# Kernel optimization log

Hardware: AMD Instinct MI355X
Metric: run time of the kernel (lower is better)

Reference implementation:

```python
import jax, jax.numpy as jnp
import numpy as np

H = 1024
IN = 512
B = 32
E_H = 0.5
Z_MIN = 0.001
Z_MAX = 0.1
DT = 1.0


def setup_inputs() -> dict:
    key = jax.random.key(0)
    ks = jax.random.split(key, 10)
    s = 1.0 / np.sqrt(H)
    uni = lambda k, shape: jax.random.uniform(k, shape, jnp.float32, -s, s)
    return {
        "x": jax.random.normal(ks[0], (IN, B), jnp.float32),
        "h": jax.random.uniform(ks[1], (B, H), jnp.float32),      # hidden state [B,H]
        "X": jnp.ones((B, H, H), jnp.float32),                     # resources
        "U": jnp.full((B, H, H), 0.9, jnp.float32),                # utilization (init 0.9)
        "c_x": uni(ks[2], (H, H)),
        "c_u": uni(ks[3], (H, H)),
        "c_U": uni(ks[4], (H, H)),
        "c_h": uni(ks[5], (H, 1)),
        "w": uni(ks[6], (H, H)),
        "p": uni(ks[7], (H, IN)),
        "b": uni(ks[8], (H, 1)),
    }


def reference(x, h, X, U, c_x, c_u, c_U, c_h, w, p, b):
    sig = jax.nn.sigmoid
    hb = h[:, :, None]                                  # h[b,j] broadcast over k -> [B,H,1]
    # resource (X) update: z_x + (1-z_x)*X - dt*U*X*h
    z_x = Z_MIN + (Z_MAX - Z_MIN) * sig(c_x)            # [H,H]
    X_new = z_x + (1.0 - z_x) * X - DT * U * (X * hb)   # [B,H,H]
    # utilization (U) update, clamped to [Ucap (detached), 1]
    z_u = Z_MIN + (Z_MAX - Z_MIN) * sig(c_u)            # [H,H]
    Ucap = 0.9 * sig(c_U)                               # [H,H]
    U_new = Ucap * z_u + (1.0 - z_u) * U + DT * Ucap * ((1.0 - U) * hb)
    U_new = jnp.clip(U_new, jax.lax.stop_gradient(Ucap), 1.0)
    # hidden update with dynamic weights W = w * U * X (per batch)
    z_h = E_H * sig(c_h)                                # [H,1]
    W = w * U_new * X_new                               # [B,H,H]
    rec = jnp.einsum("bjk,bk->jb", W, h)               # [H,B]
    pre = rec + p @ x + b                               # [H,B]
    h_newT = (1.0 - z_h) * h.T + z_h * sig(pre)         # [H,B]
    return h_newT.T                                     # [B,H]
```

## Files before the change

kernel.cpp:

```cpp
#include <hip/hip_runtime.h>

#define HH 1024
#define INW 512
#define BB 32
#define Z_MIN_C 0.001f
#define Z_RANGE_C 0.099f
#define E_H_C 0.5f

__device__ __forceinline__ float sigmoidf_(float v) {
    return 1.0f / (1.0f + __expf(-v));
}

__global__ __launch_bounds__(256) void stp_fused(
    const float* __restrict__ x,
    const float* __restrict__ h,
    const float* __restrict__ X,
    const float* __restrict__ U,
    const float* __restrict__ c_x,
    const float* __restrict__ c_u,
    const float* __restrict__ c_U,
    const float* __restrict__ c_h,
    const float* __restrict__ w,
    const float* __restrict__ p,
    const float* __restrict__ bias,
    float* __restrict__ out)
{
    const int j = blockIdx.x;
    const int t = threadIdx.x;
    const int lane = t & 63;
    const int wave = t >> 6;

    __shared__ float px_part[8][BB];
    __shared__ float rec_part[BB][4];

    {
        const int b_id = t & 31;
        const int seg = t >> 5;
        float acc = 0.0f;
        const float* prow = p + j * INW + seg * 64;
        const float* xcol = x + seg * 64 * BB + b_id;
        #pragma unroll 8
        for (int i = 0; i < 64; ++i)
            acc += prow[i] * xcol[i * BB];
        px_part[seg][b_id] = acc;
    }

    const int k0 = t * 4;
    float4 cx4 = *(const float4*)(c_x + j * HH + k0);
    float4 cu4 = *(const float4*)(c_u + j * HH + k0);
    float4 cC4 = *(const float4*)(c_U + j * HH + k0);
    float4 wv4 = *(const float4*)(w + j * HH + k0);
    const float* cxv = &cx4.x;
    const float* cuv = &cu4.x;
    const float* cCv = &cC4.x;
    const float* wvv = &wv4.x;

    float zx[4], ozx[4], Acoef[4], ozu[4], Uc[4], wr[4];
    #pragma unroll
    for (int c = 0; c < 4; ++c) {
        float zxx = Z_MIN_C + Z_RANGE_C * sigmoidf_(cxv[c]);
        float zuu = Z_MIN_C + Z_RANGE_C * sigmoidf_(cuv[c]);
        float ucc = 0.9f * sigmoidf_(cCv[c]);
        zx[c] = zxx;
        ozx[c] = 1.0f - zxx;
        ozu[c] = 1.0f - zuu;
        Uc[c] = ucc;
        Acoef[c] = ucc * zuu;
        wr[c] = wvv[c];
    }

    for (int b = 0; b < BB; ++b) {
        const float hj = h[b * HH + j];
        float4 hk4 = *(const float4*)(h + b * HH + k0);
        const int rowbase = (b * HH + j) * HH;
        float4 Xv4 = *(const float4*)(X + rowbase + k0);
        float4 Uv4 = *(const float4*)(U + rowbase + k0);
        const float* Xv = &Xv4.x;
        const float* Uv = &Uv4.x;
        const float* hk = &hk4.x;

        float s = 0.0f;
        #pragma unroll
        for (int c = 0; c < 4; ++c) {
            float Xn = fmaf(ozx[c], Xv[c], zx[c]);
            Xn = fmaf(-Uv[c], Xv[c] * hj, Xn);
            float Un = fmaf(ozu[c], Uv[c], Acoef[c]);
            Un = fmaf(Uc[c] * hj, 1.0f - Uv[c], Un);
            Un = fminf(fmaxf(Un, Uc[c]), 1.0f);
            s = fmaf(wr[c] * hk[c], Un * Xn, s);
        }

        #pragma unroll
        for (int off = 32; off > 0; off >>= 1)
            s += __shfl_xor(s, off);
        if (lane == 0) rec_part[b][wave] = s;
    }
    __syncthreads();

    if (t < BB) {
        float rec = rec_part[t][0] + rec_part[t][1] + rec_part[t][2] + rec_part[t][3];
        float px = 0.0f;
        #pragma unroll
        for (int sgi = 0; sgi < 8; ++sgi) px += px_part[sgi][t];
        float pre = rec + px + bias[j];
        float zh = E_H_C * sigmoidf_(c_h[j]);
        float hv = h[t * HH + j];
        out[t * HH + j] = (1.0f - zh) * hv + zh * sigmoidf_(pre);
    }
}

extern "C" void kernel_launch(void* const* d_in, const int* in_sizes, int n_in,
                              void* d_out, int out_size, void* d_ws, size_t ws_size,
                              hipStream_t stream) {
    const float* x   = (const float*)d_in[0];
    const float* h   = (const float*)d_in[1];
    const float* X   = (const float*)d_in[2];
    const float* U   = (const float*)d_in[3];
    const float* c_x = (const float*)d_in[4];
    const float* c_u = (const float*)d_in[5];
    const float* c_U = (const float*)d_in[6];
    const float* c_h = (const float*)d_in[7];
    const float* w   = (const float*)d_in[8];
    const float* p   = (const float*)d_in[9];
    const float* b   = (const float*)d_in[10];
    float* out = (float*)d_out;

    stp_fused<<<HH, 256, 0, stream>>>(x, h, X, U, c_x, c_u, c_U, c_h, w, p, b, out);
}
```

Baseline: 305.8 us.

## Split batch across two blocks per row and batch loads four-deep

Each output row j is now handled by two blocks, each covering half the batch (16 entries). This doubles the grid to 2048 blocks for more parallelism over the memory-bound X/U stream. The inner loop issues loads for four batch rows before computing them, raising memory-level parallelism per thread. Shuffle reductions are deferred to the end, at the cost of more registers. Sigmoid coefficient computation and the w/c loads are duplicated across the two blocks.

```diff
diff --git a/kernel.cpp b/kernel.cpp
--- a/kernel.cpp
+++ b/kernel.cpp
@@ -3,6 +3,7 @@
 #define HH 1024
 #define INW 512
 #define BB 32
+#define BG 16
 #define Z_MIN_C 0.001f
 #define Z_RANGE_C 0.099f
 #define E_H_C 0.5f
@@ -25,23 +26,24 @@
     const float* __restrict__ bias,
     float* __restrict__ out)
 {
-    const int j = blockIdx.x;
+    const int j = blockIdx.x >> 1;
+    const int g = blockIdx.x & 1;
     const int t = threadIdx.x;
     const int lane = t & 63;
     const int wave = t >> 6;
 
-    __shared__ float px_part[8][BB];
-    __shared__ float rec_part[BB][4];
+    __shared__ float px_part[16][BG];
+    __shared__ float rec_part[BG][4];
 
     {
-        const int b_id = t & 31;
-        const int seg = t >> 5;
+        const int b_id = t & 15;
+        const int seg = t >> 4;
         float acc = 0.0f;
-        const float* prow = p + j * INW + seg * 64;
-        const float* xcol = x + seg * 64 * BB + b_id;
-        #pragma unroll 8
-        for (int i = 0; i < 64; ++i)
-            acc += prow[i] * xcol[i * BB];
+        const float* prow = p + j * INW + seg * 32;
+        const float* xcol = x + seg * 32 * BB + (g * BG + b_id);
+        #pragma unroll
+        for (int i = 0; i < 32; ++i)
+            acc = fmaf(prow[i], xcol[i * BB], acc);
         px_part[seg][b_id] = acc;
     }
 
@@ -69,43 +71,62 @@
         wr[c] = wvv[c];
     }
 
-    for (int b = 0; b < BB; ++b) {
-        const float hj = h[b * HH + j];
-        float4 hk4 = *(const float4*)(h + b * HH + k0);
-        const int rowbase = (b * HH + j) * HH;
-        float4 Xv4 = *(const float4*)(X + rowbase + k0);
-        float4 Uv4 = *(const float4*)(U + rowbase + k0);
-        const float* Xv = &Xv4.x;
-        const float* Uv = &Uv4.x;
-        const float* hk = &hk4.x;
+    float s[BG];
+    #pragma unroll
+    for (int i = 0; i < BG; ++i) s[i] = 0.0f;
 
-        float s = 0.0f;
+    for (int bb = 0; bb < BG; bb += 4) {
+        float4 Xl[4], Ul[4], hk[4];
+        float hj[4];
         #pragma unroll
-        for (int c = 0; c < 4; ++c) {
-            float Xn = fmaf(ozx[c], Xv[c], zx[c]);
-            Xn = fmaf(-Uv[c], Xv[c] * hj, Xn);
-            float Un = fmaf(ozu[c], Uv[c], Acoef[c]);
-            Un = fmaf(Uc[c] * hj, 1.0f - Uv[c], Un);
-            Un = fminf(fmaxf(Un, Uc[c]), 1.0f);
-            s = fmaf(wr[c] * hk[c], Un * Xn, s);
+        for (int i = 0; i < 4; ++i) {
+            const int b = g * BG + bb + i;
+            const int rowbase = (b * HH + j) * HH;
+            Xl[i] = *(const float4*)(X + rowbase + k0);
+            Ul[i] = *(const float4*)(U + rowbase + k0);
+            hk[i] = *(const float4*)(h + b * HH + k0);
+            hj[i] = h[b * HH + j];
         }
+        #pragma unroll
+        for (int i = 0; i < 4; ++i) {
+            const float hjv = hj[i];
+            const float* Xv = &Xl[i].x;
+            const float* Uv = &Ul[i].x;
+            const float* hkv = &hk[i].x;
+            float ss = 0.0f;
+            #pragma unroll
+            for (int c = 0; c < 4; ++c) {
+                float Xn = fmaf(ozx[c], Xv[c], zx[c]);
+                Xn = fmaf(-Uv[c], Xv[c] * hjv, Xn);
+                float Un = fmaf(ozu[c], Uv[c], Acoef[c]);
+                Un = fmaf(Uc[c] * hjv, 1.0f - Uv[c], Un);
+                Un = fminf(fmaxf(Un, Uc[c]), 1.0f);
+                ss = fmaf(wr[c] * hkv[c], Un * Xn, ss);
+            }
+            s[bb + i] += ss;
+        }
+    }
 
+    #pragma unroll
+    for (int i = 0; i < BG; ++i) {
+        float v = s[i];
         #pragma unroll
         for (int off = 32; off > 0; off >>= 1)
-            s += __shfl_xor(s, off);
-        if (lane == 0) rec_part[b][wave] = s;
+            v += __shfl_xor(v, off);
+        if (lane == 0) rec_part[i][wave] = v;
     }
     __syncthreads();
 
-    if (t < BB) {
+    if (t < BG) {
+        const int b = g * BG + t;
         float rec = rec_part[t][0] + rec_part[t][1] + rec_part[t][2] + rec_part[t][3];
         float px = 0.0f;
         #pragma unroll
-        for (int sgi = 0; sgi < 8; ++sgi) px += px_part[sgi][t];
+        for (int sgi = 0; sgi < 16; ++sgi) px += px_part[sgi][t];
         float pre = rec + px + bias[j];
         float zh = E_H_C * sigmoidf_(c_h[j]);
-        float hv = h[t * HH + j];
-        out[t * HH + j] = (1.0f - zh) * hv + zh * sigmoidf_(pre);
+        float hv = h[b * HH + j];
+        out[b * HH + j] = (1.0f - zh) * hv + zh * sigmoidf_(pre);
     }
 }
 
@@ -125,5 +146,5 @@
     const float* b   = (const float*)d_in[10];
     float* out = (float*)d_out;
 
-    stp_fused<<<HH, 256, 0, stream>>>(x, h, X, U, c_x, c_u, c_U, c_h, w, p, b, out);
+    stp_fused<<<HH * 2, 256, 0, stream>>>(x, h, X, U, c_x, c_u, c_U, c_h, w, p, b, out);
 }
```

Measured after the change: 334.2 us. 9.3% more time.
